# Kernel optimization log

Measured on AMD Instinct MI355X. Metric: run time of the kernel, lower is better.

## Reference

```python
import jax, jax.numpy as jnp
import numpy as np
from jax import lax

PRE_NMS_TOPN = 2000
POST_NMS_TOPN = 1000
NMS_THRESH = 0.7
MIN_BOX_SIZE = 4.0
BBOX_XFORM_CLIP = 4.135  # log(1000/16), standard clamp on dw/dh


def setup_inputs() -> dict:
    key = jax.random.key(0)
    k1, k2, k3, k4 = jax.random.split(key, 4)
    B, N = 8, 250000
    H, W = 800, 1333
    rpn_bbox_pred = jax.random.normal(k1, (B, N, 4), jnp.float32) * 0.5
    objectness = jax.random.normal(k2, (B, N), jnp.float32)
    # realistic anchors: centers inside image, sizes in [16, 256]
    ctr = jax.random.uniform(k3, (N, 2), jnp.float32) * jnp.array([W, H], jnp.float32)
    wh = jax.random.uniform(k4, (N, 2), jnp.float32) * 240.0 + 16.0
    anchors = jnp.concatenate([ctr - 0.5 * wh, ctr + 0.5 * wh], axis=-1)
    return {"rpn_bbox_pred": rpn_bbox_pred, "objectness": objectness,
            "anchors": anchors, "height": H, "width": W}


def _decode_clip(anchors, deltas, height, width):
    # anchors (1,N,4) broadcast against deltas (B,N,4); boxes are x1,y1,x2,y2
    aw = anchors[..., 2] - anchors[..., 0]
    ah = anchors[..., 3] - anchors[..., 1]
    ax = anchors[..., 0] + 0.5 * aw
    ay = anchors[..., 1] + 0.5 * ah
    dx, dy = deltas[..., 0], deltas[..., 1]
    dw = jnp.minimum(deltas[..., 2], BBOX_XFORM_CLIP)
    dh = jnp.minimum(deltas[..., 3], BBOX_XFORM_CLIP)
    px = dx * aw + ax
    py = dy * ah + ay
    pw = jnp.exp(dw) * aw
    ph = jnp.exp(dh) * ah
    x1 = jnp.clip(px - 0.5 * pw, 0.0, float(width))
    y1 = jnp.clip(py - 0.5 * ph, 0.0, float(height))
    x2 = jnp.clip(px + 0.5 * pw, 0.0, float(width))
    y2 = jnp.clip(py + 0.5 * ph, 0.0, float(height))
    return jnp.stack([x1, y1, x2, y2], axis=-1)


def _pairwise_iou(boxes):
    # boxes (K,4) -> iou (K,K)
    x1, y1, x2, y2 = boxes[:, 0], boxes[:, 1], boxes[:, 2], boxes[:, 3]
    area = (x2 - x1) * (y2 - y1)
    iw = jnp.maximum(jnp.minimum(x2[:, None], x2[None, :]) - jnp.maximum(x1[:, None], x1[None, :]), 0.0)
    ih = jnp.maximum(jnp.minimum(y2[:, None], y2[None, :]) - jnp.maximum(y1[:, None], y1[None, :]), 0.0)
    inter = iw * ih
    return inter / (area[:, None] + area[None, :] - inter + 1e-9)


def _nms_keep(boxes, valid):
    # sequential greedy NMS over score-sorted boxes (K,4); returns keep mask (K,)
    iou = lax.stop_gradient(_pairwise_iou(boxes))
    idxs = jnp.arange(PRE_NMS_TOPN)
    def body(i, keep):
        sup = (iou[i] > NMS_THRESH) & keep[i] & (idxs > i)
        return keep & (~sup)
    return lax.fori_loop(0, PRE_NMS_TOPN, body, valid)


def _per_image(boxes, scores):
    # boxes (N,4), scores (N,)
    ws = boxes[:, 2] - boxes[:, 0]
    hs = boxes[:, 3] - boxes[:, 1]
    size_ok = (ws >= MIN_BOX_SIZE) & (hs >= MIN_BOX_SIZE)
    masked = jnp.where(size_ok, scores, -jnp.inf)
    top_s, order = lax.top_k(masked, PRE_NMS_TOPN)   # descending sort + pre-NMS topN
    top_boxes = boxes[order]                          # (PRE,4)
    valid = top_s > -jnp.inf                          # boxes surviving size filter
    keep = _nms_keep(top_boxes, valid)
    # take first POST_NMS_TOPN kept boxes in score order (fixed-shape padding)
    sel = jnp.sort(jnp.where(keep, jnp.arange(PRE_NMS_TOPN), PRE_NMS_TOPN))[:POST_NMS_TOPN]
    out_valid = sel < PRE_NMS_TOPN
    sel_c = jnp.minimum(sel, PRE_NMS_TOPN - 1)
    out = jnp.where(out_valid[:, None], top_boxes[sel_c], 0.0)
    return out, out_valid


def reference(rpn_bbox_pred, objectness, anchors, height, width):
    proposals = _decode_clip(anchors[None], rpn_bbox_pred, height, width)  # (B,N,4)
    out, valid = jax.vmap(_per_image)(proposals, objectness)
    # padded equivalent of the ragged per-image list: (B,POST,4) boxes + (B,POST) validity
    return out, valid
```

## Files before the change

### kernel.cpp

```cpp
#include <hip/hip_runtime.h>
#include <hip/hip_bf16.h>

#define NBUCK 8192
#define P1B   32
#define CAP   4096
#define TOPN  2000
#define NP2   2048
#define OUTN  1000
#define NST   64
#define NSLOT 8
#define SLOTW 2048

typedef unsigned int u32x4 __attribute__((ext_vector_type(4)));
typedef __attribute__((address_space(1))) const unsigned GUP;
typedef __attribute__((address_space(3))) unsigned LUP;

__device__ __forceinline__ float4 decode_box(const float4 a, const float4 d, float W, float H) {
    float aw = a.z - a.x;
    float ah = a.w - a.y;
    float ax = a.x + 0.5f * aw;
    float ay = a.y + 0.5f * ah;
    float dw = fminf(d.z, 4.135f);
    float dh = fminf(d.w, 4.135f);
    float px = d.x * aw + ax;
    float py = d.y * ah + ay;
    float pw = expf(dw) * aw;
    float ph = expf(dh) * ah;
    float4 r;
    r.x = fminf(fmaxf(px - 0.5f * pw, 0.0f), W);
    r.y = fminf(fmaxf(py - 0.5f * ph, 0.0f), H);
    r.z = fminf(fmaxf(px + 0.5f * pw, 0.0f), W);
    r.w = fminf(fmaxf(py + 0.5f * ph, 0.0f), H);
    return r;
}

__device__ __forceinline__ unsigned score_key(const float4 a, const float4 d, float W, float H, float s) {
    float4 b = decode_box(a, d, W, H);
    bool ok = ((b.z - b.x) >= 4.0f) && ((b.w - b.y) >= 4.0f);
    float ms = ok ? s : -INFINITY;
    unsigned u = __float_as_uint(ms);
    return (u & 0x80000000u) ? ~u : (u | 0x80000000u);
}

__global__ void k_zero(u32x4* __restrict__ hist) {
    hist[blockIdx.x * 256 + threadIdx.x] = (u32x4){0u, 0u, 0u, 0u};
}

__global__ void __launch_bounds__(1024) k_pass1(const float* __restrict__ pred,
        const float* __restrict__ obj, const float* __restrict__ anch,
        const int* __restrict__ Hp, const int* __restrict__ Wp,
        unsigned* __restrict__ keys, unsigned* __restrict__ hist,
        unsigned* __restrict__ cnt, unsigned* __restrict__ remInit, int N) {
    __shared__ unsigned h[2 * NBUCK];
    int t = threadIdx.x;
    int b = blockIdx.y, g = blockIdx.x;
    if (g == 0 && t < 64) { if (t == 0) cnt[b * 64] = 0; remInit[b * 64 + t] = 0; }
    for (int i = t; i < 2 * NBUCK; i += 1024) h[i] = 0;
    __syncthreads();
    int chunk = (N + P1B - 1) / P1B;
    int base = g * chunk;
    int end = base + chunk; if (end > N) end = N;
    float W = (float)*Wp, H = (float)*Hp;
    unsigned cp = (t & 1) ? NBUCK : 0;
    for (int n = base + t; n < end; n += 1024) {
        float4 a = ((const float4*)anch)[n];
        float4 d = ((const float4*)pred)[(size_t)b * N + n];
        float s = obj[(size_t)b * N + n];
        unsigned key = score_key(a, d, W, H, s);
        keys[(size_t)b * N + n] = key;
        atomicAdd(&h[cp + (key >> 19)], 1u);
    }
    __syncthreads();
    for (int i = t; i < NBUCK; i += 1024) {
        unsigned v = h[i] + h[NBUCK + i];
        if (v) atomicAdd(&hist[b * NBUCK + i], v);
    }
}

__global__ void k_scan(const unsigned* __restrict__ hist, unsigned* __restrict__ Lb) {
    __shared__ unsigned h[NBUCK];
    __shared__ unsigned csum[256];
    __shared__ unsigned suf[256];
    __shared__ int tcS;
    __shared__ unsigned beforeS;
    int b = blockIdx.x, t = threadIdx.x;
    const unsigned* src = hist + (size_t)b * NBUCK;
    for (int i = t * 4; i < NBUCK; i += 1024) {
        uint4 v = *(const uint4*)(src + i);
        h[i] = v.x; h[i + 1] = v.y; h[i + 2] = v.z; h[i + 3] = v.w;
    }
    if (t == 0) tcS = -1;
    __syncthreads();
    unsigned s = 0;
    for (int j = 0; j < 32; j++) s += h[t * 32 + j];
    csum[t] = s; suf[t] = s;
    __syncthreads();
    for (int d = 1; d < 256; d <<= 1) {
        unsigned v = (t + d < 256) ? suf[t + d] : 0;
        __syncthreads();
        suf[t] += v;
        __syncthreads();
    }
    if (suf[t] >= (unsigned)TOPN && (t == 255 || suf[t + 1] < (unsigned)TOPN)) {
        tcS = t; beforeS = (t == 255) ? 0u : suf[t + 1];
    }
    __syncthreads();
    if (t == 0) {
        unsigned L = 0;
        int tc = tcS;
        if (tc >= 0) {
            unsigned r = beforeS;
            for (int bkt = tc * 32 + 31;; bkt--) {
                r += h[bkt];
                if (r >= (unsigned)TOPN || bkt == tc * 32) { L = (unsigned)bkt; break; }
            }
        }
        Lb[b] = L;
    }
}

__global__ void k_collect(const unsigned* __restrict__ keys, const unsigned* __restrict__ Lb,
                          unsigned* __restrict__ count, unsigned long long* __restrict__ cand,
                          int N) {
    __shared__ unsigned lk[1024], ln[1024];
    __shared__ unsigned lcnt, lbase;
    int b = blockIdx.y, t = threadIdx.x;
    if (t == 0) lcnt = 0;
    __syncthreads();
    unsigned L = Lb[b];
    const unsigned* kb = keys + (size_t)b * N;
    int e = blockIdx.x * 256 + t;
    int n0 = e * 4;
    if (n0 + 3 < N) {
        uint4 kv = ((const uint4*)kb)[e];
        if ((kv.x >> 19) >= L) { unsigned p = atomicAdd(&lcnt, 1u); lk[p] = kv.x; ln[p] = n0; }
        if ((kv.y >> 19) >= L) { unsigned p = atomicAdd(&lcnt, 1u); lk[p] = kv.y; ln[p] = n0 + 1; }
        if ((kv.z >> 19) >= L) { unsigned p = atomicAdd(&lcnt, 1u); lk[p] = kv.z; ln[p] = n0 + 2; }
        if ((kv.w >> 19) >= L) { unsigned p = atomicAdd(&lcnt, 1u); lk[p] = kv.w; ln[p] = n0 + 3; }
    } else {
        for (int j = 0; j < 4; j++) {
            int n = n0 + j;
            if (n < N) {
                unsigned k = kb[n];
                if ((k >> 19) >= L) { unsigned p = atomicAdd(&lcnt, 1u); lk[p] = k; ln[p] = n; }
            }
        }
    }
    __syncthreads();
    if (t == 0) lbase = atomicAdd(&count[b * 64], lcnt);
    __syncthreads();
    unsigned c = lcnt, bs = lbase;
    for (unsigned i = t; i < c; i += 256) {
        unsigned pos = bs + i;
        if (pos < CAP) cand[(size_t)b * CAP + pos] =
            ((unsigned long long)lk[i] << 32) | (unsigned)(~ln[i]);
    }
}

#define REGX(e, p, d, lo)  ((lo) == (d) ? ((e) >= (p) ? (e) : (p)) : ((e) >= (p) ? (p) : (e)))

__global__ void __launch_bounds__(256) k_sort1(unsigned long long* __restrict__ cand,
        const unsigned* __restrict__ count) {
    __shared__ unsigned long long s[512];
    int b = blockIdx.x >> 3, g = blockIdx.x & 7;
    int t = threadIdx.x;
    unsigned cnt = count[b * 64]; if (cnt > CAP) cnt = CAP;
    unsigned long long* cb = cand + (size_t)b * CAP + g * 512;
    int g0 = g * 512 + t, g1 = g * 512 + t + 256;
    unsigned long long e0 = (g0 < (int)cnt) ? cb[t] : 0ULL;
    unsigned long long e1 = (g1 < (int)cnt) ? cb[t + 256] : 0ULL;

    #pragma unroll
    for (int k = 2; k <= 64; k <<= 1) {
        bool d0 = ((g0 & k) == 0);
        bool d1 = ((g1 & k) == 0);
        #pragma unroll
        for (int j = k >> 1; j >= 1; j >>= 1) {
            bool lo = ((t & j) == 0);
            unsigned long long p0 = __shfl_xor(e0, j, 64);
            unsigned long long p1 = __shfl_xor(e1, j, 64);
            e0 = REGX(e0, p0, d0, lo);
            e1 = REGX(e1, p1, d1, lo);
        }
    }
    for (int k = 128; k <= 512; k <<= 1) {
        s[t] = e0; s[t + 256] = e1;
        __syncthreads();
        for (int j = k >> 1; j >= 64; j >>= 1) {
            int i = ((t & ~(j - 1)) << 1) | (t & (j - 1));
            int l = i + j;
            bool desc = (((g * 512 + i) & k) == 0);
            unsigned long long x = s[i], y = s[l];
            if (desc ? (x < y) : (x > y)) { s[i] = y; s[l] = x; }
            __syncthreads();
        }
        e0 = s[t]; e1 = s[t + 256];
        bool d0 = ((g0 & k) == 0);
        bool d1 = ((g1 & k) == 0);
        #pragma unroll
        for (int j = 32; j >= 1; j >>= 1) {
            bool lo = ((t & j) == 0);
            unsigned long long p0 = __shfl_xor(e0, j, 64);
            unsigned long long p1 = __shfl_xor(e1, j, 64);
            e0 = REGX(e0, p0, d0, lo);
            e1 = REGX(e1, p1, d1, lo);
        }
    }
    cb[t] = e0; cb[t + 256] = e1;
}

__global__ void __launch_bounds__(1024) k_sort2(const unsigned long long* __restrict__ cand,
        const float* __restrict__ pred, const float* __restrict__ anch,
        const int* __restrict__ Hp, const int* __restrict__ Wp,
        float4* __restrict__ topbox, unsigned* __restrict__ remInit, int N) {
    __shared__ unsigned long long s[CAP];
    int b = blockIdx.x, t = threadIdx.x;
    const unsigned long long* cb = cand + (size_t)b * CAP;
    unsigned long long e0 = cb[t], e1 = cb[t + 1024], e2 = cb[t + 2048], e3 = cb[t + 3072];
    for (int k = 1024; k <= 4096; k <<= 1) {
        s[t] = e0; s[t + 1024] = e1; s[t + 2048] = e2; s[t + 3072] = e3;
        __syncthreads();
        for (int j = k >> 1; j >= 64; j >>= 1) {
            #pragma unroll
            for (int cc = 0; cc < 2; cc++) {
                int c = t + cc * 1024;
                int i = ((c & ~(j - 1)) << 1) | (c & (j - 1));
                int l = i + j;
                bool desc = ((i & k) == 0);
                unsigned long long x = s[i], y = s[l];
                if (desc ? (x < y) : (x > y)) { s[i] = y; s[l] = x; }
            }
            __syncthreads();
        }
        e0 = s[t]; e1 = s[t + 1024]; e2 = s[t + 2048]; e3 = s[t + 3072];
        bool d0 = ((t & k) == 0);
        bool d1 = (((t + 1024) & k) == 0);
        bool d2 = (((t + 2048) & k) == 0);
        bool d3 = (((t + 3072) & k) == 0);
        #pragma unroll
        for (int j = 32; j >= 1; j >>= 1) {
            bool lo = ((t & j) == 0);
            unsigned long long p0 = __shfl_xor(e0, j, 64);
            unsigned long long p1 = __shfl_xor(e1, j, 64);
            unsigned long long p2 = __shfl_xor(e2, j, 64);
            unsigned long long p3 = __shfl_xor(e3, j, 64);
            e0 = REGX(e0, p0, d0, lo);
            e1 = REGX(e1, p1, d1, lo);
            e2 = REGX(e2, p2, d2, lo);
            e3 = REGX(e3, p3, d3, lo);
        }
    }
    float W = (float)*Wp, H = (float)*Hp;
    #pragma unroll
    for (int m = 0; m < 2; m++) {
        unsigned long long v = m ? e1 : e0;
        int r = t + m * 1024;
        unsigned key = (unsigned)(v >> 32);
        bool valid = key > 0x007FFFFFu;
        float4 outb = {0.f, 0.f, 0.f, 0.f};
        if (valid) {
            unsigned idx = ~((unsigned)v);
            float4 a = ((const float4*)anch)[idx];
            float4 d = ((const float4*)pred)[(size_t)b * N + idx];
            outb = decode_box(a, d, W, H);
        }
        topbox[(size_t)b * NP2 + r] = outb;
        if (r < TOPN && !valid) atomicOr(&remInit[b * 64 + (r >> 5)], 1u << (r & 31));
    }
}

__global__ void __launch_bounds__(256) k_mask(const float4* __restrict__ topbox,
                                              unsigned* __restrict__ maskT) {
    const double MID = 23488103.0 / 33554432.0;
    __shared__ float4 bx[NP2];
    __shared__ float ar[NP2];
    int b = blockIdx.y, c = blockIdx.x;
    int t = threadIdx.x;
    int j0 = c * 32;
    for (int i = j0 + t; i < NP2; i += 256) {
        float4 v = topbox[(size_t)b * NP2 + i];
        bx[i] = v;
        ar[i] = (v.z - v.x) * (v.w - v.y);
    }
    __syncthreads();
    int r = t & 31;
    int wg = t >> 5;
    int i = j0 + r;
    float4 bi = bx[i];
    float areai = ar[i];
    unsigned* outc = maskT + ((size_t)(b * NST + c)) * SLOTW;
    for (int w = wg; w < c; w += 8) outc[w * 32 + r] = 0u;
    for (int w = c + wg; w < 64; w += 8) {
        unsigned bits = 0;
        int jbase = w * 32;
        #pragma unroll
        for (int jj = 0; jj < 32; jj++) {
            int j = jbase + jj;
            float4 bj = bx[j];
            float iw = fmaxf(fminf(bi.z, bj.z) - fmaxf(bi.x, bj.x), 0.0f);
            float ih = fmaxf(fminf(bi.w, bj.w) - fmaxf(bi.y, bj.y), 0.0f);
            float inter = iw * ih;
            float denom = areai + ar[j] - inter + 1e-9f;
            if ((double)inter >= MID * (double)denom) bits |= (1u << jj);
        }
        if (w == c) bits &= ~((2u << r) - 1u);
        outc[w * 32 + r] = bits;
    }
}

__global__ void __launch_bounds__(512) k_nms(const unsigned* __restrict__ maskT,
        const unsigned* __restrict__ remInit, const float4* __restrict__ topbox,
        float* __restrict__ out, int B) {
    __shared__ __align__(16) unsigned smbuf[NSLOT * SLOTW];
    __shared__ int ready[NST];
    __shared__ int consumed;
    __shared__ int stop;
    int b = blockIdx.x;
    int t = threadIdx.x;
    const unsigned* m = maskT + (size_t)b * NST * SLOTW;

    float4* ob = (float4*)out + (size_t)b * OUTN;
    for (int i = t; i < OUTN; i += 512) ob[i] = make_float4(0.f, 0.f, 0.f, 0.f);
    float* vout = out + (size_t)B * (OUTN * 4) + (size_t)b * OUTN;
    for (int i = t; i < OUTN; i += 512) vout[i] = 0.0f;

    if (t < NST) ready[t] = 0;
    if (t == 0) { consumed = 0; stop = 0; }
    __syncthreads();

    unsigned removed = 0xFFFFFFFFu;

    if (t >= 64) {
        int w = t >> 6;
        int lam = t & 63;
        int base = ((lam >> 3) << 5) + ((((lam & 7) ^ ((lam >> 3) & 7))) << 2);
        #pragma unroll 1
        for (int s = w - 1; s < NST; s += 7) {
            if (__hip_atomic_load(&stop, __ATOMIC_RELAXED, __HIP_MEMORY_SCOPE_WORKGROUP)) break;
            while (__hip_atomic_load(&consumed, __ATOMIC_ACQUIRE,
                   __HIP_MEMORY_SCOPE_WORKGROUP) < s - (NSLOT - 1))
                __builtin_amdgcn_s_sleep(2);
            const unsigned* gs = m + (size_t)s * SLOTW + base;
            unsigned* sl = smbuf + (s & (NSLOT - 1)) * SLOTW;
            #pragma unroll
            for (int i = 0; i < 8; i++)
                __builtin_amdgcn_global_load_lds((GUP*)(gs + i * 256),
                                                 (LUP*)(sl + i * 256), 16, 0, 0);
            asm volatile("s_waitcnt vmcnt(0)" ::: "memory");
            if (lam == 0) __hip_atomic_store(&ready[s], 1, __ATOMIC_RELEASE,
                                             __HIP_MEMORY_SCOPE_WORKGROUP);
        }
    } else {
        removed = remInit[b * 64 + t];
        if (t == 62) removed |= 0xFFFF0000u;
        if (t == 63) removed = 0xFFFFFFFFu;
        int e = t & 7;
        int keptRun = 0;
        #pragma unroll 1
        for (int s = 0; s < NST; s++) {
            while (!__hip_atomic_load(&ready[s], __ATOMIC_ACQUIRE,
                   __HIP_MEMORY_SCOPE_WORKGROUP))
                __builtin_amdgcn_s_sleep(2);
            const u32x4* sq = (const u32x4*)(smbuf + (s & (NSLOT - 1)) * SLOTW) + t * 8;
            unsigned R[32];
            #pragma unroll
            for (int k = 0; k < 8; k++) *(u32x4*)&R[k << 2] = sq[k ^ e];
            __builtin_amdgcn_sched_group_barrier(0x100, 8, 0);
            unsigned alive = ~__builtin_amdgcn_readlane(removed, s);
            unsigned Is[32];
            #pragma unroll
            for (int q = 0; q < 32; q++) Is[q] = __builtin_amdgcn_readlane(R[q], s);
            #pragma unroll
            for (int q = 0; q < 32; q++) alive &= ~(((alive >> q) & 1u) ? Is[q] : 0u);
            unsigned a0 = 0, a1 = 0, a2 = 0, a3 = 0;
            #pragma unroll
            for (int q = 0; q < 32; q += 4) {
                a0 |= ((alive >> q) & 1u)       ? R[q]     : 0u;
                a1 |= ((alive >> (q + 1)) & 1u) ? R[q + 1] : 0u;
                a2 |= ((alive >> (q + 2)) & 1u) ? R[q + 2] : 0u;
                a3 |= ((alive >> (q + 3)) & 1u) ? R[q + 3] : 0u;
            }
            removed |= (a0 | a1) | (a2 | a3);
            keptRun += __popc(~__builtin_amdgcn_readlane(removed, s));
            if (keptRun >= OUTN) {
                if (t == 0) {
                    __hip_atomic_store(&stop, 1, __ATOMIC_RELAXED, __HIP_MEMORY_SCOPE_WORKGROUP);
                    __hip_atomic_store(&consumed, NST, __ATOMIC_RELEASE, __HIP_MEMORY_SCOPE_WORKGROUP);
                }
                break;
            }
            if (t == 0) __hip_atomic_store(&consumed, s + 1, __ATOMIC_RELEASE,
                                           __HIP_MEMORY_SCOPE_WORKGROUP);
        }
        unsigned keep = ~removed;
        int cnt = __popc(keep);
        int ex = cnt;
        for (int off = 1; off < 64; off <<= 1) {
            int v = __shfl_up(ex, off, 64);
            if (t >= off) ex += v;
        }
        ex -= cnt;
        int pos = ex;
        for (int j = 0; j < 32; j++) {
            if ((keep >> j) & 1u) {
                if (pos < OUTN) {
                    float4 bxv = topbox[(size_t)b * NP2 + t * 32 + j];
                    ob[pos] = bxv;
                    vout[pos] = 1.0f;
                }
                pos++;
            }
        }
    }
}

extern "C" void kernel_launch(void* const* d_in, const int* in_sizes, int n_in,
                              void* d_out, int out_size, void* d_ws, size_t ws_size,
                              hipStream_t stream) {
    const float* pred = (const float*)d_in[0];
    const float* obj  = (const float*)d_in[1];
    const float* anch = (const float*)d_in[2];
    const int* Hp = (const int*)d_in[3];
    const int* Wp = (const int*)d_in[4];
    int N = in_sizes[2] / 4;
    int B = in_sizes[1] / N;

    char* ws = (char*)d_ws;
    size_t off = 0;
    auto take = [&](size_t bytes) { void* p = ws + off; off = (off + bytes + 255) & ~(size_t)255; return p; };

    size_t regA_bytes = (size_t)B * N * 4;
    size_t mask_bytes = (size_t)B * NST * SLOTW * 4;
    char* regA = (char*)take(regA_bytes > mask_bytes ? regA_bytes : mask_bytes);
    unsigned* keys  = (unsigned*)regA;
    unsigned* maskT = (unsigned*)regA;
    unsigned* hist           = (unsigned*)take((size_t)B * NBUCK * 4);
    unsigned long long* cand = (unsigned long long*)take((size_t)B * CAP * 8);
    float4* topbox           = (float4*)take((size_t)B * NP2 * 16);
    unsigned* cnt            = (unsigned*)take((size_t)B * 64 * 4);
    unsigned* Lb             = (unsigned*)take((size_t)B * 64 * 4);
    unsigned* remInit        = (unsigned*)take((size_t)B * 64 * 4);

    k_zero   <<<(B * NBUCK) / 1024, 256, 0, stream>>>((u32x4*)hist);
    k_pass1  <<<dim3(P1B, B), 1024, 0, stream>>>(pred, obj, anch, Hp, Wp, keys, hist, cnt, remInit, N);
    k_scan   <<<B, 256, 0, stream>>>(hist, Lb);
    k_collect<<<dim3((N + 1023) / 1024, B), 256, 0, stream>>>(keys, Lb, cnt, cand, N);
    k_sort1  <<<B * 8, 256, 0, stream>>>(cand, cnt);
    k_sort2  <<<B, 1024, 0, stream>>>(cand, pred, anch, Hp, Wp, topbox, remInit, N);
    k_mask   <<<dim3(NST, B), 256, 0, stream>>>(topbox, maskT);
    k_nms    <<<B, 512, 0, stream>>>(maskT, remInit, topbox, (float*)d_out, B);
}
```

Measured before the change: 123.0 us.

## Skip empty sort chunks, use a 2048-wide merge when few candidates, balance mask blocks

In k_sort1, chunks lying wholly beyond the candidate count now write zeros and exit without sorting. k_sort2 reads the count and, when it is at most 2048, runs a 2048-element merge with half the shared-memory passes instead of the full 4096 bitonic merge. k_mask pairs triangle row c with row 63-c in one block, halving the grid and evening out per-block work. The intent is to cut wasted sort work and the tail imbalance of the triangular mask computation. The cost is branch complexity, and the 2048 path is only correct if the zero-padded tail stays sorted.

Result: faster. 118.2 us (-3.9%).

```diff
diff --git a/kernel.cpp b/kernel.cpp
--- a/kernel.cpp
+++ b/kernel.cpp
@@ -166,6 +166,10 @@
     int t = threadIdx.x;
     unsigned cnt = count[b * 64]; if (cnt > CAP) cnt = CAP;
     unsigned long long* cb = cand + (size_t)b * CAP + g * 512;
+    if ((unsigned)(g * 512) >= cnt) {
+        cb[t] = 0ULL; cb[t + 256] = 0ULL;
+        return;
+    }
     int g0 = g * 512 + t, g1 = g * 512 + t + 256;
     unsigned long long e0 = (g0 < (int)cnt) ? cb[t] : 0ULL;
     unsigned long long e1 = (g1 < (int)cnt) ? cb[t + 256] : 0ULL;
@@ -210,45 +214,76 @@
 }
 
 __global__ void __launch_bounds__(1024) k_sort2(const unsigned long long* __restrict__ cand,
+        const unsigned* __restrict__ count,
         const float* __restrict__ pred, const float* __restrict__ anch,
         const int* __restrict__ Hp, const int* __restrict__ Wp,
         float4* __restrict__ topbox, unsigned* __restrict__ remInit, int N) {
     __shared__ unsigned long long s[CAP];
     int b = blockIdx.x, t = threadIdx.x;
     const unsigned long long* cb = cand + (size_t)b * CAP;
-    unsigned long long e0 = cb[t], e1 = cb[t + 1024], e2 = cb[t + 2048], e3 = cb[t + 3072];
-    for (int k = 1024; k <= 4096; k <<= 1) {
-        s[t] = e0; s[t + 1024] = e1; s[t + 2048] = e2; s[t + 3072] = e3;
-        __syncthreads();
-        for (int j = k >> 1; j >= 64; j >>= 1) {
-            #pragma unroll
-            for (int cc = 0; cc < 2; cc++) {
-                int c = t + cc * 1024;
-                int i = ((c & ~(j - 1)) << 1) | (c & (j - 1));
+    unsigned cnt = count[b * 64]; if (cnt > CAP) cnt = CAP;
+    unsigned long long e0, e1;
+    if (cnt <= 2048) {
+        e0 = cb[t]; e1 = cb[t + 1024];
+        for (int k = 1024; k <= 2048; k <<= 1) {
+            s[t] = e0; s[t + 1024] = e1;
+            __syncthreads();
+            for (int j = k >> 1; j >= 64; j >>= 1) {
+                int i = ((t & ~(j - 1)) << 1) | (t & (j - 1));
                 int l = i + j;
                 bool desc = ((i & k) == 0);
                 unsigned long long x = s[i], y = s[l];
                 if (desc ? (x < y) : (x > y)) { s[i] = y; s[l] = x; }
-            }
+                __syncthreads();
+            }
+            e0 = s[t]; e1 = s[t + 1024];
+            bool d0 = ((t & k) == 0);
+            bool d1 = (((t + 1024) & k) == 0);
+            #pragma unroll
+            for (int j = 32; j >= 1; j >>= 1) {
+                bool lo = ((t & j) == 0);
+                unsigned long long p0 = __shfl_xor(e0, j, 64);
+                unsigned long long p1 = __shfl_xor(e1, j, 64);
+                e0 = REGX(e0, p0, d0, lo);
+                e1 = REGX(e1, p1, d1, lo);
+            }
+        }
+    } else {
+        unsigned long long f0 = cb[t], f1 = cb[t + 1024], f2 = cb[t + 2048], f3 = cb[t + 3072];
+        for (int k = 1024; k <= 4096; k <<= 1) {
+            s[t] = f0; s[t + 1024] = f1; s[t + 2048] = f2; s[t + 3072] = f3;
             __syncthreads();
-        }
-        e0 = s[t]; e1 = s[t + 1024]; e2 = s[t + 2048]; e3 = s[t + 3072];
-        bool d0 = ((t & k) == 0);
-        bool d1 = (((t + 1024) & k) == 0);
-        bool d2 = (((t + 2048) & k) == 0);
-        bool d3 = (((t + 3072) & k) == 0);
-        #pragma unroll
-        for (int j = 32; j >= 1; j >>= 1) {
-            bool lo = ((t & j) == 0);
-            unsigned long long p0 = __shfl_xor(e0, j, 64);
-            unsigned long long p1 = __shfl_xor(e1, j, 64);
-            unsigned long long p2 = __shfl_xor(e2, j, 64);
-            unsigned long long p3 = __shfl_xor(e3, j, 64);
-            e0 = REGX(e0, p0, d0, lo);
-            e1 = REGX(e1, p1, d1, lo);
-            e2 = REGX(e2, p2, d2, lo);
-            e3 = REGX(e3, p3, d3, lo);
-        }
+            for (int j = k >> 1; j >= 64; j >>= 1) {
+                #pragma unroll
+                for (int cc = 0; cc < 2; cc++) {
+                    int c = t + cc * 1024;
+                    int i = ((c & ~(j - 1)) << 1) | (c & (j - 1));
+                    int l = i + j;
+                    bool desc = ((i & k) == 0);
+                    unsigned long long x = s[i], y = s[l];
+                    if (desc ? (x < y) : (x > y)) { s[i] = y; s[l] = x; }
+                }
+                __syncthreads();
+            }
+            f0 = s[t]; f1 = s[t + 1024]; f2 = s[t + 2048]; f3 = s[t + 3072];
+            bool d0 = ((t & k) == 0);
+            bool d1 = (((t + 1024) & k) == 0);
+            bool d2 = (((t + 2048) & k) == 0);
+            bool d3 = (((t + 3072) & k) == 0);
+            #pragma unroll
+            for (int j = 32; j >= 1; j >>= 1) {
+                bool lo = ((t & j) == 0);
+                unsigned long long p0 = __shfl_xor(f0, j, 64);
+                unsigned long long p1 = __shfl_xor(f1, j, 64);
+                unsigned long long p2 = __shfl_xor(f2, j, 64);
+                unsigned long long p3 = __shfl_xor(f3, j, 64);
+                f0 = REGX(f0, p0, d0, lo);
+                f1 = REGX(f1, p1, d1, lo);
+                f2 = REGX(f2, p2, d2, lo);
+                f3 = REGX(f3, p3, d3, lo);
+            }
+        }
+        e0 = f0; e1 = f1;
     }
     float W = (float)*Wp, H = (float)*Hp;
     #pragma unroll
@@ -274,9 +309,9 @@
     const double MID = 23488103.0 / 33554432.0;
     __shared__ float4 bx[NP2];
     __shared__ float ar[NP2];
-    int b = blockIdx.y, c = blockIdx.x;
+    int b = blockIdx.y, cp = blockIdx.x;
     int t = threadIdx.x;
-    int j0 = c * 32;
+    int j0 = cp * 32;
     for (int i = j0 + t; i < NP2; i += 256) {
         float4 v = topbox[(size_t)b * NP2 + i];
         bx[i] = v;
@@ -285,26 +320,30 @@
     __syncthreads();
     int r = t & 31;
     int wg = t >> 5;
-    int i = j0 + r;
-    float4 bi = bx[i];
-    float areai = ar[i];
-    unsigned* outc = maskT + ((size_t)(b * NST + c)) * SLOTW;
-    for (int w = wg; w < c; w += 8) outc[w * 32 + r] = 0u;
-    for (int w = c + wg; w < 64; w += 8) {
-        unsigned bits = 0;
-        int jbase = w * 32;
-        #pragma unroll
-        for (int jj = 0; jj < 32; jj++) {
-            int j = jbase + jj;
-            float4 bj = bx[j];
-            float iw = fmaxf(fminf(bi.z, bj.z) - fmaxf(bi.x, bj.x), 0.0f);
-            float ih = fmaxf(fminf(bi.w, bj.w) - fmaxf(bi.y, bj.y), 0.0f);
-            float inter = iw * ih;
-            float denom = areai + ar[j] - inter + 1e-9f;
-            if ((double)inter >= MID * (double)denom) bits |= (1u << jj);
-        }
-        if (w == c) bits &= ~((2u << r) - 1u);
-        outc[w * 32 + r] = bits;
+    #pragma unroll
+    for (int half = 0; half < 2; half++) {
+        int c = half ? (63 - cp) : cp;
+        int i = c * 32 + r;
+        float4 bi = bx[i];
+        float areai = ar[i];
+        unsigned* outc = maskT + ((size_t)(b * NST + c)) * SLOTW;
+        for (int w = wg; w < c; w += 8) outc[w * 32 + r] = 0u;
+        for (int w = c + wg; w < 64; w += 8) {
+            unsigned bits = 0;
+            int jbase = w * 32;
+            #pragma unroll
+            for (int jj = 0; jj < 32; jj++) {
+                int j = jbase + jj;
+                float4 bj = bx[j];
+                float iw = fmaxf(fminf(bi.z, bj.z) - fmaxf(bi.x, bj.x), 0.0f);
+                float ih = fmaxf(fminf(bi.w, bj.w) - fmaxf(bi.y, bj.y), 0.0f);
+                float inter = iw * ih;
+                float denom = areai + ar[j] - inter + 1e-9f;
+                if ((double)inter >= MID * (double)denom) bits |= (1u << jj);
+            }
+            if (w == c) bits &= ~((2u << r) - 1u);
+            outc[w * 32 + r] = bits;
+        }
     }
 }
 
@@ -446,7 +485,7 @@
     k_scan   <<<B, 256, 0, stream>>>(hist, Lb);
     k_collect<<<dim3((N + 1023) / 1024, B), 256, 0, stream>>>(keys, Lb, cnt, cand, N);
     k_sort1  <<<B * 8, 256, 0, stream>>>(cand, cnt);
-    k_sort2  <<<B, 1024, 0, stream>>>(cand, pred, anch, Hp, Wp, topbox, remInit, N);
-    k_mask   <<<dim3(NST, B), 256, 0, stream>>>(topbox, maskT);
+    k_sort2  <<<B, 1024, 0, stream>>>(cand, cnt, pred, anch, Hp, Wp, topbox, remInit, N);
+    k_mask   <<<dim3(32, B), 256, 0, stream>>>(topbox, maskT);
     k_nms    <<<B, 512, 0, stream>>>(maskT, remInit, topbox, (float*)d_out, B);
 }
```
